# Kernel optimization log

Measured on AMD Instinct MI355X. Metric: run time of the kernel, lower is better.

## Reference

```python
import jax, jax.numpy as jnp
import numpy as np

B, N, H, D = 8, 1024, 16, 64
HD = H * D

def setup_inputs() -> dict:
    key = jax.random.key(0)
    ks = jax.random.split(key, 7)
    return {
        "hidden_states": jax.random.normal(ks[0], (B, N, HD), dtype=jnp.float32),
        "qkv_w": jax.random.normal(ks[1], (3 * HD, HD), dtype=jnp.float32) * (HD ** -0.5),
        "q_bias": jax.random.normal(ks[2], (1, 1, HD), dtype=jnp.float32) * 0.02,
        "v_bias": jax.random.normal(ks[3], (1, 1, HD), dtype=jnp.float32) * 0.02,
        "rel_pos": jax.random.normal(ks[4], (1, H, N, N), dtype=jnp.float32),
        "rel_2d_pos": jax.random.normal(ks[5], (1, H, N, N), dtype=jnp.float32),
        "attention_mask": jax.random.randint(ks[6], (B, 1, 1, N), 0, 2, dtype=jnp.int32),
    }

def reference(hidden_states, qkv_w, q_bias, v_bias, rel_pos, rel_2d_pos, attention_mask):
    # fast_qkv path: fused projection, no bias in linear, then add q/v biases
    qkv = jnp.einsum("bnh,oh->bno", hidden_states, qkv_w)  # [B,N,3*HD]
    q, k, v = jnp.split(qkv, 3, axis=-1)
    q = q + q_bias
    v = v + v_bias

    def to_heads(x):  # [B,N,HD] -> [B,H,N,D]
        return x.reshape(B, N, H, D).transpose(0, 2, 1, 3)

    qh = to_heads(q) / jnp.sqrt(jnp.float32(D))
    kh = to_heads(k)
    vh = to_heads(v)

    scores = jnp.einsum("bhnd,bhmd->bhnm", qh, kh)  # [B,H,N,N]
    scores = scores + rel_pos + rel_2d_pos
    # torch mask_fill_ with value 1e-8 (NOT -inf) where mask is True
    scores = jnp.where(attention_mask.astype(bool), jnp.float32(1e-8), scores)
    probs = jax.nn.softmax(scores.astype(jnp.float32), axis=-1).astype(vh.dtype)
    # dropout prob = 0.0 (eval): identity
    ctx = jnp.einsum("bhnm,bhmd->bhnd", probs, vh)  # [B,H,N,D]
    ctx = ctx.transpose(0, 2, 1, 3).reshape(B, N, HD)
    return ctx
```

## Files before the change

### kernel.cpp

```cpp
#include <hip/hip_runtime.h>


typedef __bf16 bf16;
typedef __bf16 bf16x8 __attribute__((ext_vector_type(8)));
typedef __bf16 bf16x4 __attribute__((ext_vector_type(4)));
typedef float floatx4 __attribute__((ext_vector_type(4)));

#define MFMA16(a, b, c) __builtin_amdgcn_mfma_f32_16x16x32_bf16((a), (b), (c), 0, 0, 0)

#define LOG2E 1.4426950408889634f

__device__ __forceinline__ void gld16(const bf16* g, bf16* l) {
    __builtin_amdgcn_global_load_lds(
        (const __attribute__((address_space(1))) unsigned int*)g,
        (__attribute__((address_space(3))) unsigned int*)l, 16, 0, 0);
}

__global__ __launch_bounds__(256) void cvt_kernel(const float* __restrict__ x,
                                                  bf16* __restrict__ y, int n4) {
    int i = blockIdx.x * blockDim.x + threadIdx.x;
    if (i >= n4) return;
    float4 v = ((const float4*)x)[i];
    bf16x4 o;
    o.x = (bf16)v.x; o.y = (bf16)v.y; o.z = (bf16)v.z; o.w = (bf16)v.w;
    ((bf16x4*)y)[i] = o;
}

__global__ __launch_bounds__(256) void combine_kernel(const float* __restrict__ a,
                                                      const float* __restrict__ b,
                                                      bf16* __restrict__ y, int n4) {
    int i = blockIdx.x * blockDim.x + threadIdx.x;
    if (i >= n4) return;
    float4 va = ((const float4*)a)[i];
    float4 vb = ((const float4*)b)[i];
    bf16x4 o;
    o.x = (bf16)((va.x + vb.x) * LOG2E); o.y = (bf16)((va.y + vb.y) * LOG2E);
    o.z = (bf16)((va.z + vb.z) * LOG2E); o.w = (bf16)((va.w + vb.w) * LOG2E);
    ((bf16x4*)y)[i] = o;
}

__global__ __launch_bounds__(256) void mask_kernel(const int* __restrict__ m,
                                                   float* __restrict__ om, int n) {
    int i = blockIdx.x * blockDim.x + threadIdx.x;
    if (i < n) om[i] = m[i] ? 0.f : 1.f;
}

__global__ __launch_bounds__(256) void qkv_gemm(
    const bf16* __restrict__ X, const bf16* __restrict__ W,
    const float* __restrict__ qbias, const float* __restrict__ vbias,
    bf16* __restrict__ qbuf, bf16* __restrict__ kbuf, bf16* __restrict__ vbuf) {
    __shared__ __align__(16) bf16 Al[128 * 32];
    __shared__ __align__(16) bf16 Bl[128 * 32];

    int tid = threadIdx.x, lane = tid & 63, w = tid >> 6;
    int quad = lane >> 4, lcol = lane & 15;
    int bx = blockIdx.x;
    int by = blockIdx.y;
    int wr = w >> 1, wc = w & 1;

    floatx4 z4 = {0.f, 0.f, 0.f, 0.f};
    floatx4 acc[4][4];
    for (int i = 0; i < 4; ++i)
        for (int j = 0; j < 4; ++j) acc[i][j] = z4;

    const bf16* Ag = X + (size_t)by * 128 * 1024;
    const bf16* Bg = W + (size_t)bx * 128 * 1024;

    for (int kt = 0; kt < 32; ++kt) {
        int k0 = kt * 32;
        __syncthreads();
        for (int j = 0; j < 2; ++j) {
            int c = (w * 2 + j) * 64 + lane;
            int row = c >> 2;
            int dc = (c & 3) ^ (row & 3);
            gld16(Ag + (size_t)row * 1024 + k0 + dc * 8, &Al[(w * 2 + j) * 64 * 8]);
        }
        for (int j = 0; j < 2; ++j) {
            int c = (w * 2 + j) * 64 + lane;
            int row = c >> 2;
            int dc = (c & 3) ^ (row & 3);
            gld16(Bg + (size_t)row * 1024 + k0 + dc * 8, &Bl[(w * 2 + j) * 64 * 8]);
        }
        __syncthreads();

        bf16x8 af[4], bfr[4];
        for (int i = 0; i < 4; ++i) {
            int r = wr * 64 + i * 16 + lcol;
            af[i] = *(const bf16x8*)&Al[r * 32 + ((quad ^ (r & 3)) * 8)];
        }
        for (int j = 0; j < 4; ++j) {
            int r = wc * 64 + j * 16 + lcol;
            bfr[j] = *(const bf16x8*)&Bl[r * 32 + ((quad ^ (r & 3)) * 8)];
        }
        for (int i = 0; i < 4; ++i)
            for (int j = 0; j < 4; ++j) acc[i][j] = MFMA16(af[i], bfr[j], acc[i][j]);
    }

    int col0 = bx * 128 + wc * 64;
    int row0 = by * 128 + wr * 64;
    int seg = col0 >> 10;

    for (int i = 0; i < 4; ++i) {
        int m0 = row0 + i * 16 + quad * 4;
        int bb = m0 >> 10, n0 = m0 & 1023;
        for (int j = 0; j < 4; ++j) {
            int o = col0 + j * 16 + lcol;
            if (seg == 0) {
                int hh = o >> 6, d = o & 63;
                float qb = qbias[o];
                for (int r = 0; r < 4; ++r) {
                    float v = (acc[i][j][r] + qb) * (0.125f * LOG2E);
                    qbuf[((size_t)((bb * 16 + hh) * 1024 + n0 + r)) * 64 + d] = (bf16)v;
                }
            } else if (seg == 1) {
                int o2 = o - 1024;
                int hh = o2 >> 6, d = o2 & 63;
                for (int r = 0; r < 4; ++r) {
                    kbuf[((size_t)((bb * 16 + hh) * 1024 + n0 + r)) * 64 + d] = (bf16)acc[i][j][r];
                }
            } else {
                int o2 = o - 2048;
                int hh = o2 >> 6, d = o2 & 63;
                float vbv = vbias[o2];
                bf16x4 pk;
                pk.x = (bf16)(acc[i][j][0] + vbv);
                pk.y = (bf16)(acc[i][j][1] + vbv);
                pk.z = (bf16)(acc[i][j][2] + vbv);
                pk.w = (bf16)(acc[i][j][3] + vbv);
                *(bf16x4*)&vbuf[((size_t)((bb * 16 + hh) * 64 + d)) * 1024 + n0] = pk;
            }
        }
    }
}

__global__ __launch_bounds__(256, 3) void flash_attn(
    const bf16* __restrict__ qbuf, const bf16* __restrict__ kbuf,
    const bf16* __restrict__ vbuf, const bf16* __restrict__ bias,
    const float* __restrict__ om, float* __restrict__ out) {
    __shared__ __align__(16) bf16 Kl[2][64 * 64];
    __shared__ __align__(16) bf16 Vl[2][64 * 64];
    __shared__ __align__(16) bf16 Pl[4][2][16 * 72];

    int tid = threadIdx.x, lane = tid & 63, w = tid >> 6;
    int quad = lane >> 4, lcol = lane & 15;
    int bx = blockIdx.x;
    int b = bx & 7, h = (bx >> 3) & 15, q2 = bx >> 7;

    const bf16* kb = kbuf + ((size_t)((b * 16 + h) * 1024)) * 64;
    const bf16* vb = vbuf + ((size_t)((b * 16 + h) * 64)) * 1024;
    const float* omb = om + b * 1024;

    int qrow[2] = {q2 * 128 + w * 16, q2 * 128 + 64 + w * 16};
    bf16x8 qf[2][2];
    const bf16* bb[2];
#pragma unroll
    for (int s = 0; s < 2; ++s) {
        const bf16* qp = qbuf + ((size_t)((b * 16 + h) * 1024 + qrow[s] + lcol)) * 64;
        qf[s][0] = *(const bf16x8*)(qp + quad * 8);
        qf[s][1] = *(const bf16x8*)(qp + 32 + quad * 8);
        bb[s] = bias + (size_t)h * 1024 * 1024 + (size_t)(qrow[s] + lcol) * 1024;
    }

    floatx4 z4 = {0.f, 0.f, 0.f, 0.f};
    floatx4 oacc[2][4];
    float lrun[2] = {0.f, 0.f};
#pragma unroll
    for (int s = 0; s < 2; ++s)
        for (int j = 0; j < 4; ++j) oacc[s][j] = z4;

#pragma unroll
    for (int j = 0; j < 2; ++j) {
        int c = (w * 2 + j) * 64 + lane;
        int key = c >> 3;
        int dc = (c & 7) ^ (key & 7);
        gld16(kb + (size_t)key * 64 + dc * 8, &Kl[0][(w * 2 + j) * 512]);
    }
#pragma unroll
    for (int j = 0; j < 2; ++j) {
        int c = (w * 2 + j) * 64 + lane;
        int d = c >> 3;
        int kc = (c & 7) ^ (d & 7);
        gld16(vb + (size_t)d * 1024 + kc * 8, &Vl[0][(w * 2 + j) * 512]);
    }

    bf16x4 bf_[2][4];
    floatx4 of_[4];
#pragma unroll
    for (int j = 0; j < 4; ++j) {
#pragma unroll
        for (int s = 0; s < 2; ++s) bf_[s][j] = *(const bf16x4*)(bb[s] + j * 16 + quad * 4);
        of_[j] = *(const floatx4*)(omb + j * 16 + quad * 4);
    }

    for (int kt = 0; kt < 16; ++kt) {
        int k0 = kt * 64;
        int cur = kt & 1, nxt = cur ^ 1;
        __syncthreads();

        if (kt < 15) {
            int k1 = k0 + 64;
#pragma unroll
            for (int j = 0; j < 2; ++j) {
                int c = (w * 2 + j) * 64 + lane;
                int key = c >> 3;
                int dc = (c & 7) ^ (key & 7);
                gld16(kb + (size_t)(k1 + key) * 64 + dc * 8, &Kl[nxt][(w * 2 + j) * 512]);
            }
#pragma unroll
            for (int j = 0; j < 2; ++j) {
                int c = (w * 2 + j) * 64 + lane;
                int d = c >> 3;
                int kc = (c & 7) ^ (d & 7);
                gld16(vb + (size_t)d * 1024 + k1 + kc * 8, &Vl[nxt][(w * 2 + j) * 512]);
            }
        }
        int kp = (kt < 15) ? k0 + 64 : 0;
        bf16x4 bn[2][4];
        floatx4 on[4];
#pragma unroll
        for (int j = 0; j < 4; ++j) {
#pragma unroll
            for (int s = 0; s < 2; ++s) bn[s][j] = *(const bf16x4*)(bb[s] + kp + j * 16 + quad * 4);
            on[j] = *(const floatx4*)(omb + kp + j * 16 + quad * 4);
        }

        floatx4 sacc[2][4];
#pragma unroll
        for (int j = 0; j < 4; ++j) {
            int key = j * 16 + lcol;
            bf16x8 kf0 = *(const bf16x8*)&Kl[cur][key * 64 + ((quad ^ (key & 7)) * 8)];
            bf16x8 kf1 = *(const bf16x8*)&Kl[cur][key * 64 + (((4 + quad) ^ (key & 7)) * 8)];
#pragma unroll
            for (int s = 0; s < 2; ++s) {
                floatx4 binit;
                binit[0] = (float)bf_[s][j][0]; binit[1] = (float)bf_[s][j][1];
                binit[2] = (float)bf_[s][j][2]; binit[3] = (float)bf_[s][j][3];
                sacc[s][j] = MFMA16(kf0, qf[s][0], binit);
                sacc[s][j] = MFMA16(kf1, qf[s][1], sacc[s][j]);
            }
        }

        float p[2][4][4];
#pragma unroll
        for (int s = 0; s < 2; ++s) {
            float psum = 0.f;
#pragma unroll
            for (int j = 0; j < 4; ++j)
#pragma unroll
                for (int r = 0; r < 4; ++r) {
                    float sv = fmaf(sacc[s][j][r], of_[j][r], 1e-8f * LOG2E);
                    p[s][j][r] = __builtin_amdgcn_exp2f(sv);
                    psum += p[s][j][r];
                }
            lrun[s] += psum;
        }

#pragma unroll
        for (int s = 0; s < 2; ++s)
#pragma unroll
            for (int j = 0; j < 4; ++j) {
                bf16x4 pk;
                pk.x = (bf16)p[s][j][0]; pk.y = (bf16)p[s][j][1];
                pk.z = (bf16)p[s][j][2]; pk.w = (bf16)p[s][j][3];
                *(bf16x4*)&Pl[w][s][lcol * 72 + j * 16 + quad * 4] = pk;
            }
        bf16x8 pf0[2], pf1[2];
#pragma unroll
        for (int s = 0; s < 2; ++s) {
            pf0[s] = *(const bf16x8*)&Pl[w][s][lcol * 72 + quad * 8];
            pf1[s] = *(const bf16x8*)&Pl[w][s][lcol * 72 + 32 + quad * 8];
        }

#pragma unroll
        for (int jd = 0; jd < 4; ++jd) {
            int dd = jd * 16 + lcol;
            bf16x8 vf0 = *(const bf16x8*)&Vl[cur][dd * 64 + ((quad ^ (dd & 7)) * 8)];
            bf16x8 vf1 = *(const bf16x8*)&Vl[cur][dd * 64 + (((4 + quad) ^ (dd & 7)) * 8)];
            oacc[0][jd] = MFMA16(vf0, pf0[0], oacc[0][jd]);
            oacc[1][jd] = MFMA16(vf0, pf0[1], oacc[1][jd]);
            oacc[0][jd] = MFMA16(vf1, pf1[0], oacc[0][jd]);
            oacc[1][jd] = MFMA16(vf1, pf1[1], oacc[1][jd]);
        }

#pragma unroll
        for (int j = 0; j < 4; ++j) {
#pragma unroll
            for (int s = 0; s < 2; ++s) bf_[s][j] = bn[s][j];
            of_[j] = on[j];
        }
    }

#pragma unroll
    for (int s = 0; s < 2; ++s) {
        float l = lrun[s];
        l += __shfl_xor(l, 16);
        l += __shfl_xor(l, 32);
        float linv = 1.f / l;
#pragma unroll
        for (int jd = 0; jd < 4; ++jd) {
            float4 st;
            st.x = oacc[s][jd][0] * linv;
            st.y = oacc[s][jd][1] * linv;
            st.z = oacc[s][jd][2] * linv;
            st.w = oacc[s][jd][3] * linv;
            *(float4*)&out[((size_t)(b * 1024 + qrow[s] + lcol)) * 1024 + h * 64 + jd * 16 + quad * 4] = st;
        }
    }
}

extern "C" void kernel_launch(void* const* d_in, const int* in_sizes, int n_in,
                              void* d_out, int out_size, void* d_ws, size_t ws_size,
                              hipStream_t stream) {
    const float* hs   = (const float*)d_in[0];
    const float* qkvw = (const float*)d_in[1];
    const float* qb   = (const float*)d_in[2];
    const float* vbi  = (const float*)d_in[3];
    const float* rel  = (const float*)d_in[4];
    const float* rel2 = (const float*)d_in[5];
    const int*   msk  = (const int*)d_in[6];
    float* out = (float*)d_out;

    char* w = (char*)d_ws;
    bf16* Xb = (bf16*)w;  w += (size_t)8388608 * 2;
    bf16* Wb = (bf16*)w;  w += (size_t)3145728 * 2;
    bf16* Bb = (bf16*)w;  w += (size_t)16777216 * 2;
    bf16* Qb = (bf16*)w;  w += (size_t)8388608 * 2;
    bf16* Kb = (bf16*)w;  w += (size_t)8388608 * 2;
    bf16* Vb = (bf16*)w;  w += (size_t)8388608 * 2;
    float* OM = (float*)w; w += (size_t)8192 * 4;

    cvt_kernel<<<8388608 / 4 / 256, 256, 0, stream>>>(hs, Xb, 8388608 / 4);
    cvt_kernel<<<3145728 / 4 / 256, 256, 0, stream>>>(qkvw, Wb, 3145728 / 4);
    combine_kernel<<<16777216 / 4 / 256, 256, 0, stream>>>(rel, rel2, Bb, 16777216 / 4);
    mask_kernel<<<32, 256, 0, stream>>>(msk, OM, 8192);
    qkv_gemm<<<dim3(24, 64), 256, 0, stream>>>(Xb, Wb, qb, vbi, Qb, Kb, Vb);
    flash_attn<<<1024, 256, 0, stream>>>(Qb, Kb, Vb, Bb, OM, out);
}
```

Baseline: 383.2 us.

## Keep softmax probabilities in registers via permuted key order, remap block-to-XCD scheduling

Permutes the key ordering inside each 64-key tile so the S-accumulator register layout of the QK^T MFMA matches the B-operand layout needed for the PV MFMA. This lets P be packed directly from registers instead of round-tripping through LDS. The K swizzle is changed to match the new access pattern, and the bias and mask loads use the permuted offsets. Removing the P LDS buffer lets launch bounds rise to 5 blocks per CU, and the block index is remapped so blocks sharing a head and query chunk land on the same XCD for L2 reuse of the bias. The risks are extra register pressure under the higher occupancy target and a correctness dependence on the permutation matching exactly.

```diff
diff --git a/kernel.cpp b/kernel.cpp
--- a/kernel.cpp
+++ b/kernel.cpp
@@ -9,6 +9,8 @@
 #define MFMA16(a, b, c) __builtin_amdgcn_mfma_f32_16x16x32_bf16((a), (b), (c), 0, 0, 0)
 
 #define LOG2E 1.4426950408889634f
+
+#define GK(key) ((((key) ^ ((key) >> 3)) & 3) | (((((key) >> 2) ^ ((key) >> 3)) & 1) << 2))
 
 __device__ __forceinline__ void gld16(const bf16* g, bf16* l) {
     __builtin_amdgcn_global_load_lds(
@@ -133,18 +135,20 @@
     }
 }
 
-__global__ __launch_bounds__(256, 3) void flash_attn(
+__global__ __launch_bounds__(256, 5) void flash_attn(
     const bf16* __restrict__ qbuf, const bf16* __restrict__ kbuf,
     const bf16* __restrict__ vbuf, const bf16* __restrict__ bias,
     const float* __restrict__ om, float* __restrict__ out) {
     __shared__ __align__(16) bf16 Kl[2][64 * 64];
     __shared__ __align__(16) bf16 Vl[2][64 * 64];
-    __shared__ __align__(16) bf16 Pl[4][2][16 * 72];
 
     int tid = threadIdx.x, lane = tid & 63, w = tid >> 6;
     int quad = lane >> 4, lcol = lane & 15;
     int bx = blockIdx.x;
-    int b = bx & 7, h = (bx >> 3) & 15, q2 = bx >> 7;
+    int xcd = bx & 7, slot = bx >> 3;
+    int pair = xcd * 16 + (slot >> 3);
+    int b = slot & 7;
+    int h = pair >> 3, q2 = pair & 7;
 
     const bf16* kb = kbuf + ((size_t)((b * 16 + h) * 1024)) * 64;
     const bf16* vb = vbuf + ((size_t)((b * 16 + h) * 64)) * 1024;
@@ -172,7 +176,7 @@
     for (int j = 0; j < 2; ++j) {
         int c = (w * 2 + j) * 64 + lane;
         int key = c >> 3;
-        int dc = (c & 7) ^ (key & 7);
+        int dc = (c & 7) ^ GK(key);
         gld16(kb + (size_t)key * 64 + dc * 8, &Kl[0][(w * 2 + j) * 512]);
     }
 #pragma unroll
@@ -187,9 +191,10 @@
     floatx4 of_[4];
 #pragma unroll
     for (int j = 0; j < 4; ++j) {
-#pragma unroll
-        for (int s = 0; s < 2; ++s) bf_[s][j] = *(const bf16x4*)(bb[s] + j * 16 + quad * 4);
-        of_[j] = *(const floatx4*)(omb + j * 16 + quad * 4);
+        int kboff = ((j >> 1) << 5) + (quad << 3) + ((j & 1) << 2);
+#pragma unroll
+        for (int s = 0; s < 2; ++s) bf_[s][j] = *(const bf16x4*)(bb[s] + kboff);
+        of_[j] = *(const floatx4*)(omb + kboff);
     }
 
     for (int kt = 0; kt < 16; ++kt) {
@@ -203,7 +208,7 @@
             for (int j = 0; j < 2; ++j) {
                 int c = (w * 2 + j) * 64 + lane;
                 int key = c >> 3;
-                int dc = (c & 7) ^ (key & 7);
+                int dc = (c & 7) ^ GK(key);
                 gld16(kb + (size_t)(k1 + key) * 64 + dc * 8, &Kl[nxt][(w * 2 + j) * 512]);
             }
 #pragma unroll
@@ -219,17 +224,19 @@
         floatx4 on[4];
 #pragma unroll
         for (int j = 0; j < 4; ++j) {
-#pragma unroll
-            for (int s = 0; s < 2; ++s) bn[s][j] = *(const bf16x4*)(bb[s] + kp + j * 16 + quad * 4);
-            on[j] = *(const floatx4*)(omb + kp + j * 16 + quad * 4);
+            int kboff = ((j >> 1) << 5) + (quad << 3) + ((j & 1) << 2);
+#pragma unroll
+            for (int s = 0; s < 2; ++s) bn[s][j] = *(const bf16x4*)(bb[s] + kp + kboff);
+            on[j] = *(const floatx4*)(omb + kp + kboff);
         }
 
         floatx4 sacc[2][4];
 #pragma unroll
         for (int j = 0; j < 4; ++j) {
-            int key = j * 16 + lcol;
-            bf16x8 kf0 = *(const bf16x8*)&Kl[cur][key * 64 + ((quad ^ (key & 7)) * 8)];
-            bf16x8 kf1 = *(const bf16x8*)&Kl[cur][key * 64 + (((4 + quad) ^ (key & 7)) * 8)];
+            int key = ((j >> 1) << 5) + ((lcol >> 2) << 3) + ((j & 1) << 2) + (lcol & 3);
+            int gk = GK(key);
+            bf16x8 kf0 = *(const bf16x8*)&Kl[cur][key * 64 + ((quad ^ gk) * 8)];
+            bf16x8 kf1 = *(const bf16x8*)&Kl[cur][key * 64 + (((4 + quad) ^ gk) * 8)];
 #pragma unroll
             for (int s = 0; s < 2; ++s) {
                 floatx4 binit;
@@ -255,20 +262,17 @@
             lrun[s] += psum;
         }
 
-#pragma unroll
-        for (int s = 0; s < 2; ++s)
-#pragma unroll
-            for (int j = 0; j < 4; ++j) {
-                bf16x4 pk;
-                pk.x = (bf16)p[s][j][0]; pk.y = (bf16)p[s][j][1];
-                pk.z = (bf16)p[s][j][2]; pk.w = (bf16)p[s][j][3];
-                *(bf16x4*)&Pl[w][s][lcol * 72 + j * 16 + quad * 4] = pk;
-            }
         bf16x8 pf0[2], pf1[2];
 #pragma unroll
         for (int s = 0; s < 2; ++s) {
-            pf0[s] = *(const bf16x8*)&Pl[w][s][lcol * 72 + quad * 8];
-            pf1[s] = *(const bf16x8*)&Pl[w][s][lcol * 72 + 32 + quad * 8];
+            pf0[s][0] = (bf16)p[s][0][0]; pf0[s][1] = (bf16)p[s][0][1];
+            pf0[s][2] = (bf16)p[s][0][2]; pf0[s][3] = (bf16)p[s][0][3];
+            pf0[s][4] = (bf16)p[s][1][0]; pf0[s][5] = (bf16)p[s][1][1];
+            pf0[s][6] = (bf16)p[s][1][2]; pf0[s][7] = (bf16)p[s][1][3];
+            pf1[s][0] = (bf16)p[s][2][0]; pf1[s][1] = (bf16)p[s][2][1];
+            pf1[s][2] = (bf16)p[s][2][2]; pf1[s][3] = (bf16)p[s][2][3];
+            pf1[s][4] = (bf16)p[s][3][0]; pf1[s][5] = (bf16)p[s][3][1];
+            pf1[s][6] = (bf16)p[s][3][2]; pf1[s][7] = (bf16)p[s][3][3];
         }
 
 #pragma unroll
```

After: 550.2 us. 1.44x slower.
